# Optimization experiments

Measured on AMD Instinct MI355X. Metric: run time of the kernel, lower is better.

Reference implementation:

```python
import jax, jax.numpy as jnp
import numpy as np

EPS = 1e-5

def layer_norm(x, gamma, beta):
    mu = jnp.mean(x, axis=-1, keepdims=True)
    var = jnp.mean((x - mu) ** 2, axis=-1, keepdims=True)
    return (x - mu) * jax.lax.rsqrt(var + EPS) * gamma + beta

def setup_inputs() -> dict:
    key = jax.random.key(0)
    ks = jax.random.split(key, 12)
    N, E, D, B = 100000, 1200000, 64, 1
    x_h = jax.random.normal(ks[0], (N, D), dtype=jnp.float32)
    edge_index = jax.random.randint(ks[1], (2, E), 0, N, dtype=jnp.int64)
    edge_attr_h = jax.random.normal(ks[2], (E, D), dtype=jnp.float32)
    u = jax.random.normal(ks[3], (B, 1), dtype=jnp.float32)
    batch = jnp.zeros((N,), dtype=jnp.int64)
    s = 0.05
    W1 = jax.random.normal(ks[4], (2 * D, D), dtype=jnp.float32) * s
    b1 = jnp.zeros((D,), dtype=jnp.float32)
    g1 = jnp.ones((D,), dtype=jnp.float32); be1 = jnp.zeros((D,), dtype=jnp.float32)
    W2 = jax.random.normal(ks[5], (2 * D + 1, D), dtype=jnp.float32) * s
    b2 = jnp.zeros((D,), dtype=jnp.float32)
    g2 = jnp.ones((D,), dtype=jnp.float32); be2 = jnp.zeros((D,), dtype=jnp.float32)
    W3 = jax.random.normal(ks[6], (D, D), dtype=jnp.float32) * s
    b3 = jnp.zeros((D,), dtype=jnp.float32)
    g3 = jnp.ones((D,), dtype=jnp.float32); be3 = jnp.zeros((D,), dtype=jnp.float32)
    return {"x_h": x_h, "edge_index": edge_index, "edge_attr_h": edge_attr_h, "u": u, "batch": batch,
            "W1": W1, "b1": b1, "g1": g1, "be1": be1,
            "W2": W2, "b2": b2, "g2": g2, "be2": be2,
            "W3": W3, "b3": b3, "g3": g3, "be3": be3}

def reference(x_h, edge_index, edge_attr_h, u, batch,
              W1, b1, g1, be1, W2, b2, g2, be2, W3, b3, g3, be3):
    N = x_h.shape[0]
    row, col = edge_index[0], edge_index[1]
    # gather source node features, concat with edge features -> mlp1
    m = jnp.concatenate([x_h[row], edge_attr_h], axis=1)            # [E, 2D]
    m = layer_norm(jax.nn.relu(m @ W1 + b1), g1, be1)               # [E, D]
    # scatter_mean over destination nodes
    summed = jax.ops.segment_sum(m, col, num_segments=N)            # [N, D]
    cnt = jax.ops.segment_sum(jnp.ones((m.shape[0],), m.dtype), col, num_segments=N)
    agg = summed / jnp.maximum(cnt, 1.0)[:, None]                   # [N, D]
    h = jnp.concatenate([x_h, agg, u[batch]], axis=1)               # [N, 2D+1]
    h = layer_norm(jax.nn.relu(h @ W2 + b2), g2, be2)
    h = layer_norm(h @ W3 + b3, g3, be3)
    return h + x_h
```

## Files before the change

### kernel.cpp

```cpp
#include <hip/hip_runtime.h>

#define EPS 1e-5f

typedef __attribute__((ext_vector_type(8))) short short8v;
typedef __attribute__((ext_vector_type(4))) float f32x4;

__device__ __forceinline__ unsigned short f2bf(float f) {
    unsigned u = __builtin_bit_cast(unsigned, f);
    u += 0x7fffu + ((u >> 16) & 1u);
    return (unsigned short)(u >> 16);
}

__global__ __launch_bounds__(256) void zero_kernel(float* __restrict__ p, long n) {
    long i = (long)blockIdx.x * blockDim.x + threadIdx.x;
    long stride = (long)gridDim.x * blockDim.x;
    long n4 = n >> 2;
    float4* p4 = (float4*)p;
    for (long k = i; k < n4; k += stride) p4[k] = make_float4(0.f, 0.f, 0.f, 0.f);
    for (long k = (n4 << 2) + i; k < n; k += stride) p[k] = 0.f;
}

__global__ __launch_bounds__(256) void edge_kernel(
    const float* __restrict__ x_h, const int* __restrict__ eidx,
    const float* __restrict__ eattr,
    const float* __restrict__ W1, const float* __restrict__ b1,
    const float* __restrict__ g1, const float* __restrict__ be1,
    float* __restrict__ summed, float* __restrict__ cnt,
    int E, int N)
{
    const int lane = threadIdx.x & 63;
    const int wid  = threadIdx.x >> 6;
    const int c = lane & 15;
    const int q = lane >> 4;

    short8v w1f[4][4];
    #pragma unroll
    for (int ks = 0; ks < 4; ++ks) {
        #pragma unroll
        for (int nt = 0; nt < 4; ++nt) {
            int k0 = ks * 32 + q * 8;
            int n  = nt * 16 + c;
            short8v f;
            #pragma unroll
            for (int j = 0; j < 8; ++j) f[j] = (short)f2bf(W1[(k0 + j) * 64 + n]);
            w1f[ks][nt] = f;
        }
    }
    float b1v[4], g1v[4], bev[4];
    #pragma unroll
    for (int nt = 0; nt < 4; ++nt) {
        b1v[nt] = b1[nt * 16 + c];
        g1v[nt] = g1[nt * 16 + c];
        bev[nt] = be1[nt * 16 + c];
    }

    for (long e0 = (long)blockIdx.x * 256 + wid * 64; e0 < E; e0 += (long)gridDim.x * 256) {
        {
            long el = e0 + lane;
            if (el < E) atomicAdd(&cnt[eidx[E + el]], 1.f);
        }

        f32x4 acc[4][4];
        #pragma unroll
        for (int mt = 0; mt < 4; ++mt)
            #pragma unroll
            for (int nt = 0; nt < 4; ++nt)
                acc[mt][nt] = (f32x4){0.f, 0.f, 0.f, 0.f};

        #pragma unroll
        for (int mt = 0; mt < 4; ++mt) {
            long er = e0 + mt * 16 + c;
            long ec = (er < E) ? er : (E - 1);
            int src = eidx[ec];
            const float* xp = x_h + (long)src * 64;
            const float* ep = eattr + ec * 64;
            #pragma unroll
            for (int ks = 0; ks < 4; ++ks) {
                int k0 = ks * 32 + q * 8;
                const float* base = (ks < 2) ? (xp + k0) : (ep + (k0 - 64));
                float4 lo = *(const float4*)(base);
                float4 hi = *(const float4*)(base + 4);
                short8v a;
                a[0] = (short)f2bf(lo.x); a[1] = (short)f2bf(lo.y);
                a[2] = (short)f2bf(lo.z); a[3] = (short)f2bf(lo.w);
                a[4] = (short)f2bf(hi.x); a[5] = (short)f2bf(hi.y);
                a[6] = (short)f2bf(hi.z); a[7] = (short)f2bf(hi.w);
                #pragma unroll
                for (int nt = 0; nt < 4; ++nt)
                    acc[mt][nt] = __builtin_amdgcn_mfma_f32_16x16x32_bf16(
                        a, w1f[ks][nt], acc[mt][nt], 0, 0, 0);
            }
        }

        #pragma unroll
        for (int mt = 0; mt < 4; ++mt) {
            float s1[4] = {0, 0, 0, 0}, s2[4] = {0, 0, 0, 0};
            #pragma unroll
            for (int nt = 0; nt < 4; ++nt) {
                #pragma unroll
                for (int r = 0; r < 4; ++r) {
                    float f = fmaxf(acc[mt][nt][r] + b1v[nt], 0.f);
                    acc[mt][nt][r] = f;
                    s1[r] += f; s2[r] += f * f;
                }
            }
            #pragma unroll
            for (int m = 1; m <= 8; m <<= 1) {
                #pragma unroll
                for (int r = 0; r < 4; ++r) {
                    s1[r] += __shfl_xor(s1[r], m);
                    s2[r] += __shfl_xor(s2[r], m);
                }
            }
            float mu[4], rs[4]; int dst[4];
            #pragma unroll
            for (int r = 0; r < 4; ++r) {
                mu[r] = s1[r] * (1.f / 64.f);
                float var = s2[r] * (1.f / 64.f) - mu[r] * mu[r];
                rs[r] = rsqrtf(var + EPS);
                long er = e0 + mt * 16 + q * 4 + r;
                dst[r] = (er < E) ? eidx[E + er] : -1;
            }
            #pragma unroll
            for (int nt = 0; nt < 4; ++nt) {
                #pragma unroll
                for (int r = 0; r < 4; ++r) {
                    if (dst[r] >= 0) {
                        float outv = (acc[mt][nt][r] - mu[r]) * rs[r] * g1v[nt] + bev[nt];
                        atomicAdd(&summed[(long)dst[r] * 64 + nt * 16 + c], outv);
                    }
                }
            }
        }
    }
}

__global__ __launch_bounds__(256) void node_kernel(
    const float* __restrict__ x_h, const float* __restrict__ u,
    const float* __restrict__ W2, const float* __restrict__ b2,
    const float* __restrict__ g2, const float* __restrict__ be2,
    const float* __restrict__ W3, const float* __restrict__ b3,
    const float* __restrict__ g3, const float* __restrict__ be3,
    const float* __restrict__ summed, const float* __restrict__ cnt,
    float* __restrict__ out, int N)
{
    __shared__ unsigned short sh[4][64][72];

    const int lane = threadIdx.x & 63;
    const int wid  = threadIdx.x >> 6;
    const int c = lane & 15;
    const int q = lane >> 4;
    const float u0 = u[0];

    short8v w2f[4][4], w3f[2][4];
    #pragma unroll
    for (int ks = 0; ks < 4; ++ks)
        #pragma unroll
        for (int nt = 0; nt < 4; ++nt) {
            int k0 = ks * 32 + q * 8;
            int n  = nt * 16 + c;
            short8v f;
            #pragma unroll
            for (int j = 0; j < 8; ++j) f[j] = (short)f2bf(W2[(k0 + j) * 64 + n]);
            w2f[ks][nt] = f;
        }
    #pragma unroll
    for (int ks = 0; ks < 2; ++ks)
        #pragma unroll
        for (int nt = 0; nt < 4; ++nt) {
            int k0 = ks * 32 + q * 8;
            int n  = nt * 16 + c;
            short8v f;
            #pragma unroll
            for (int j = 0; j < 8; ++j) f[j] = (short)f2bf(W3[(k0 + j) * 64 + n]);
            w3f[ks][nt] = f;
        }

    float b2p[4], g2v[4], be2v[4], b3v[4], g3v[4], be3v[4];
    #pragma unroll
    for (int nt = 0; nt < 4; ++nt) {
        int n = nt * 16 + c;
        b2p[nt] = b2[n] + u0 * W2[128 * 64 + n];
        g2v[nt] = g2[n]; be2v[nt] = be2[n];
        b3v[nt] = b3[n]; g3v[nt] = g3[n]; be3v[nt] = be3[n];
    }

    const long n0 = ((long)blockIdx.x * 4 + wid) * 64;
    if (n0 >= N) return;

    #pragma unroll
    for (int mt = 0; mt < 4; ++mt) {
        long nr = n0 + mt * 16 + c;
        long nc = (nr < N) ? nr : (N - 1);
        const float* xp = x_h + nc * 64;
        const float* sp = summed + nc * 64;
        float inv = 1.f / fmaxf(cnt[nc], 1.f);

        f32x4 acc[4];
        #pragma unroll
        for (int nt = 0; nt < 4; ++nt) acc[nt] = (f32x4){0.f, 0.f, 0.f, 0.f};

        #pragma unroll
        for (int ks = 0; ks < 4; ++ks) {
            int k0 = ks * 32 + q * 8;
            short8v a;
            if (ks < 2) {
                float4 lo = *(const float4*)(xp + k0);
                float4 hi = *(const float4*)(xp + k0 + 4);
                a[0] = (short)f2bf(lo.x); a[1] = (short)f2bf(lo.y);
                a[2] = (short)f2bf(lo.z); a[3] = (short)f2bf(lo.w);
                a[4] = (short)f2bf(hi.x); a[5] = (short)f2bf(hi.y);
                a[6] = (short)f2bf(hi.z); a[7] = (short)f2bf(hi.w);
            } else {
                float4 lo = *(const float4*)(sp + k0 - 64);
                float4 hi = *(const float4*)(sp + k0 - 60);
                a[0] = (short)f2bf(lo.x * inv); a[1] = (short)f2bf(lo.y * inv);
                a[2] = (short)f2bf(lo.z * inv); a[3] = (short)f2bf(lo.w * inv);
                a[4] = (short)f2bf(hi.x * inv); a[5] = (short)f2bf(hi.y * inv);
                a[6] = (short)f2bf(hi.z * inv); a[7] = (short)f2bf(hi.w * inv);
            }
            #pragma unroll
            for (int nt = 0; nt < 4; ++nt)
                acc[nt] = __builtin_amdgcn_mfma_f32_16x16x32_bf16(a, w2f[ks][nt], acc[nt], 0, 0, 0);
        }

        float s1[4] = {0, 0, 0, 0}, s2[4] = {0, 0, 0, 0};
        #pragma unroll
        for (int nt = 0; nt < 4; ++nt)
            #pragma unroll
            for (int r = 0; r < 4; ++r) {
                float f = fmaxf(acc[nt][r] + b2p[nt], 0.f);
                acc[nt][r] = f;
                s1[r] += f; s2[r] += f * f;
            }
        #pragma unroll
        for (int m = 1; m <= 8; m <<= 1)
            #pragma unroll
            for (int r = 0; r < 4; ++r) {
                s1[r] += __shfl_xor(s1[r], m);
                s2[r] += __shfl_xor(s2[r], m);
            }
        #pragma unroll
        for (int r = 0; r < 4; ++r) {
            float mu = s1[r] * (1.f / 64.f);
            float var = s2[r] * (1.f / 64.f) - mu * mu;
            float rs = rsqrtf(var + EPS);
            #pragma unroll
            for (int nt = 0; nt < 4; ++nt) {
                float h2 = (acc[nt][r] - mu) * rs * g2v[nt] + be2v[nt];
                sh[wid][mt * 16 + q * 4 + r][nt * 16 + c] = f2bf(h2);
            }
        }
    }

    #pragma unroll
    for (int mt = 0; mt < 4; ++mt) {
        f32x4 acc[4];
        #pragma unroll
        for (int nt = 0; nt < 4; ++nt) acc[nt] = (f32x4){0.f, 0.f, 0.f, 0.f};

        #pragma unroll
        for (int ks = 0; ks < 2; ++ks) {
            short8v a = *(const short8v*)&sh[wid][mt * 16 + c][ks * 32 + q * 8];
            #pragma unroll
            for (int nt = 0; nt < 4; ++nt)
                acc[nt] = __builtin_amdgcn_mfma_f32_16x16x32_bf16(a, w3f[ks][nt], acc[nt], 0, 0, 0);
        }

        float s1[4] = {0, 0, 0, 0}, s2[4] = {0, 0, 0, 0};
        #pragma unroll
        for (int nt = 0; nt < 4; ++nt)
            #pragma unroll
            for (int r = 0; r < 4; ++r) {
                float f = acc[nt][r] + b3v[nt];
                acc[nt][r] = f;
                s1[r] += f; s2[r] += f * f;
            }
        #pragma unroll
        for (int m = 1; m <= 8; m <<= 1)
            #pragma unroll
            for (int r = 0; r < 4; ++r) {
                s1[r] += __shfl_xor(s1[r], m);
                s2[r] += __shfl_xor(s2[r], m);
            }
        #pragma unroll
        for (int r = 0; r < 4; ++r) {
            float mu = s1[r] * (1.f / 64.f);
            float var = s2[r] * (1.f / 64.f) - mu * mu;
            float rs = rsqrtf(var + EPS);
            long node = n0 + mt * 16 + q * 4 + r;
            if (node < N) {
                #pragma unroll
                for (int nt = 0; nt < 4; ++nt) {
                    long off = node * 64 + nt * 16 + c;
                    float h3 = (acc[nt][r] - mu) * rs * g3v[nt] + be3v[nt];
                    out[off] = h3 + x_h[off];
                }
            }
        }
    }
}

extern "C" void kernel_launch(void* const* d_in, const int* in_sizes, int n_in,
                              void* d_out, int out_size, void* d_ws, size_t ws_size,
                              hipStream_t stream)
{
    const float* x_h   = (const float*)d_in[0];
    const int*   eidx  = (const int*)  d_in[1];
    const float* eattr = (const float*)d_in[2];
    const float* u     = (const float*)d_in[3];
    const float* W1  = (const float*)d_in[5];
    const float* b1  = (const float*)d_in[6];
    const float* g1  = (const float*)d_in[7];
    const float* be1 = (const float*)d_in[8];
    const float* W2  = (const float*)d_in[9];
    const float* b2  = (const float*)d_in[10];
    const float* g2  = (const float*)d_in[11];
    const float* be2 = (const float*)d_in[12];
    const float* W3  = (const float*)d_in[13];
    const float* b3  = (const float*)d_in[14];
    const float* g3  = (const float*)d_in[15];
    const float* be3 = (const float*)d_in[16];

    const int N = in_sizes[0] / 64;
    const int E = in_sizes[1] / 2;

    float* summed = (float*)d_ws;
    float* cnt    = summed + (size_t)N * 64;

    long zn = (long)N * 64 + N;
    zero_kernel<<<1024, 256, 0, stream>>>(summed, zn);

    edge_kernel<<<2048, 256, 0, stream>>>(x_h, eidx, eattr, W1, b1, g1, be1,
                                          summed, cnt, E, N);

    int nblocks = (N + 255) / 256;
    node_kernel<<<nblocks, 256, 0, stream>>>(x_h, u, W2, b2, g2, be2, W3, b3, g3, be3,
                                             summed, cnt, (float*)d_out, N);
}
```

Measured before the change: 380.1 us.

## Accumulate scatter sums in bf16 with packed atomic adds

The per-node segment-sum buffer changes from fp32 to bf16. Edge results are now scattered with global_atomic_pk_add_bf16, where each even lane packs its value with its neighbour's, so there are half as many atomics and half the atomic memory traffic. The edge MFMA accumulators are also restructured so each m-tile is computed and reduced before the next starts, which lowers register pressure. The cost is accuracy: on average about 12 edges land on each node, and summing them in bf16 adds rounding error that could approach the tolerance.

```diff
diff --git a/kernel.cpp b/kernel.cpp
--- a/kernel.cpp
+++ b/kernel.cpp
@@ -9,6 +9,9 @@
     unsigned u = __builtin_bit_cast(unsigned, f);
     u += 0x7fffu + ((u >> 16) & 1u);
     return (unsigned short)(u >> 16);
+}
+__device__ __forceinline__ float bf2f(unsigned short h) {
+    return __builtin_bit_cast(float, (unsigned)h << 16);
 }
 
 __global__ __launch_bounds__(256) void zero_kernel(float* __restrict__ p, long n) {
@@ -25,7 +28,7 @@
     const float* __restrict__ eattr,
     const float* __restrict__ W1, const float* __restrict__ b1,
     const float* __restrict__ g1, const float* __restrict__ be1,
-    float* __restrict__ summed, float* __restrict__ cnt,
+    unsigned short* __restrict__ summed, float* __restrict__ cnt,
     int E, int N)
 {
     const int lane = threadIdx.x & 63;
@@ -60,13 +63,6 @@
             if (el < E) atomicAdd(&cnt[eidx[E + el]], 1.f);
         }
 
-        f32x4 acc[4][4];
-        #pragma unroll
-        for (int mt = 0; mt < 4; ++mt)
-            #pragma unroll
-            for (int nt = 0; nt < 4; ++nt)
-                acc[mt][nt] = (f32x4){0.f, 0.f, 0.f, 0.f};
-
         #pragma unroll
         for (int mt = 0; mt < 4; ++mt) {
             long er = e0 + mt * 16 + c;
@@ -74,6 +70,11 @@
             int src = eidx[ec];
             const float* xp = x_h + (long)src * 64;
             const float* ep = eattr + ec * 64;
+
+            f32x4 acc[4];
+            #pragma unroll
+            for (int nt = 0; nt < 4; ++nt) acc[nt] = (f32x4){0.f, 0.f, 0.f, 0.f};
+
             #pragma unroll
             for (int ks = 0; ks < 4; ++ks) {
                 int k0 = ks * 32 + q * 8;
@@ -87,20 +88,17 @@
                 a[6] = (short)f2bf(hi.z); a[7] = (short)f2bf(hi.w);
                 #pragma unroll
                 for (int nt = 0; nt < 4; ++nt)
-                    acc[mt][nt] = __builtin_amdgcn_mfma_f32_16x16x32_bf16(
-                        a, w1f[ks][nt], acc[mt][nt], 0, 0, 0);
-            }
-        }
-
-        #pragma unroll
-        for (int mt = 0; mt < 4; ++mt) {
+                    acc[nt] = __builtin_amdgcn_mfma_f32_16x16x32_bf16(
+                        a, w1f[ks][nt], acc[nt], 0, 0, 0);
+            }
+
             float s1[4] = {0, 0, 0, 0}, s2[4] = {0, 0, 0, 0};
             #pragma unroll
             for (int nt = 0; nt < 4; ++nt) {
                 #pragma unroll
                 for (int r = 0; r < 4; ++r) {
-                    float f = fmaxf(acc[mt][nt][r] + b1v[nt], 0.f);
-                    acc[mt][nt][r] = f;
+                    float f = fmaxf(acc[nt][r] + b1v[nt], 0.f);
+                    acc[nt][r] = f;
                     s1[r] += f; s2[r] += f * f;
                 }
             }
@@ -118,16 +116,21 @@
                 mu[r] = s1[r] * (1.f / 64.f);
                 float var = s2[r] * (1.f / 64.f) - mu[r] * mu[r];
                 rs[r] = rsqrtf(var + EPS);
-                long er = e0 + mt * 16 + q * 4 + r;
-                dst[r] = (er < E) ? eidx[E + er] : -1;
+                long er2 = e0 + mt * 16 + q * 4 + r;
+                dst[r] = (er2 < E) ? eidx[E + er2] : -1;
             }
             #pragma unroll
             for (int nt = 0; nt < 4; ++nt) {
                 #pragma unroll
                 for (int r = 0; r < 4; ++r) {
-                    if (dst[r] >= 0) {
-                        float outv = (acc[mt][nt][r] - mu[r]) * rs[r] * g1v[nt] + bev[nt];
-                        atomicAdd(&summed[(long)dst[r] * 64 + nt * 16 + c], outv);
+                    float outv = (acc[nt][r] - mu[r]) * rs[r] * g1v[nt] + bev[nt];
+                    float nb = __shfl_xor(outv, 1);
+                    if (dst[r] >= 0 && !(c & 1)) {
+                        unsigned pk = (unsigned)f2bf(outv) | ((unsigned)f2bf(nb) << 16);
+                        unsigned long long a64 = (unsigned long long)
+                            (summed + (long)dst[r] * 64 + nt * 16 + c);
+                        asm volatile("global_atomic_pk_add_bf16 %0, %1, off"
+                                     :: "v"(a64), "v"(pk) : "memory");
                     }
                 }
             }
@@ -141,7 +144,7 @@
     const float* __restrict__ g2, const float* __restrict__ be2,
     const float* __restrict__ W3, const float* __restrict__ b3,
     const float* __restrict__ g3, const float* __restrict__ be3,
-    const float* __restrict__ summed, const float* __restrict__ cnt,
+    const unsigned short* __restrict__ summed, const float* __restrict__ cnt,
     float* __restrict__ out, int N)
 {
     __shared__ unsigned short sh[4][64][72];
@@ -193,7 +196,7 @@
         long nr = n0 + mt * 16 + c;
         long nc = (nr < N) ? nr : (N - 1);
         const float* xp = x_h + nc * 64;
-        const float* sp = summed + nc * 64;
+        const unsigned short* sp = summed + nc * 64;
         float inv = 1.f / fmaxf(cnt[nc], 1.f);
 
         f32x4 acc[4];
@@ -212,12 +215,10 @@
                 a[4] = (short)f2bf(hi.x); a[5] = (short)f2bf(hi.y);
                 a[6] = (short)f2bf(hi.z); a[7] = (short)f2bf(hi.w);
             } else {
-                float4 lo = *(const float4*)(sp + k0 - 64);
-                float4 hi = *(const float4*)(sp + k0 - 60);
-                a[0] = (short)f2bf(lo.x * inv); a[1] = (short)f2bf(lo.y * inv);
-                a[2] = (short)f2bf(lo.z * inv); a[3] = (short)f2bf(lo.w * inv);
-                a[4] = (short)f2bf(hi.x * inv); a[5] = (short)f2bf(hi.y * inv);
-                a[6] = (short)f2bf(hi.z * inv); a[7] = (short)f2bf(hi.w * inv);
+                short8v raw = *(const short8v*)(sp + (k0 - 64));
+                #pragma unroll
+                for (int j = 0; j < 8; ++j)
+                    a[j] = (short)f2bf(bf2f((unsigned short)raw[j]) * inv);
             }
             #pragma unroll
             for (int nt = 0; nt < 4; ++nt)
@@ -325,11 +326,11 @@
     const int N = in_sizes[0] / 64;
     const int E = in_sizes[1] / 2;
 
-    float* summed = (float*)d_ws;
-    float* cnt    = summed + (size_t)N * 64;
-
-    long zn = (long)N * 64 + N;
-    zero_kernel<<<1024, 256, 0, stream>>>(summed, zn);
+    unsigned short* summed = (unsigned short*)d_ws;
+    float* cnt = (float*)((char*)d_ws + (size_t)N * 128);
+
+    long zn = (long)N * 32 + N;
+    zero_kernel<<<1024, 256, 0, stream>>>((float*)d_ws, zn);
 
     edge_kernel<<<2048, 256, 0, stream>>>(x_h, eidx, eattr, W1, b1, g1, be1,
                                           summed, cnt, E, N);
```

Result: faster. 364.4 us (-4.1%).
